# Kernel optimization log

Hardware: AMD Instinct MI355X
Metric: run time of the kernel (lower is better)

The kernel has to match this reference:

```python
import jax, jax.numpy as jnp
import numpy as np

# Faithful math: AlphaLayer(maxdim=1) builds the Delaunay complex with simplex
# filtration value = max pairwise Euclidean distance; BarcodePolyFeature(0, 2, 0)
# sums (death - birth)^2 over FINITE H0 bars. For this filtration, H0 births are
# all 0 and finite H0 deaths are exactly the Euclidean-MST edge lengths (the EMST
# is a subgraph of the Delaunay graph), so the feature equals
# sum over MST edges of squared edge length. We compute it with a vectorized
# Prim's algorithm (lax.scan over N-1 selection steps, vmapped over batch).

NCC = 2  # num_connected_components
EPS = 1e-8


def _batch_normalize(x):
    # per-sample, per-channel standardization over the points axis
    mu = x.mean(axis=1, keepdims=True)
    sd = x.std(axis=1, keepdims=True)
    return (x - mu) / (sd + EPS)


def _pairwise_sq(pts):
    # pts: [N, D] -> [N, N] squared Euclidean distances
    sq = jnp.sum(pts * pts, axis=-1)
    d2 = sq[:, None] + sq[None, :] - 2.0 * (pts @ pts.T)
    return jnp.maximum(d2, 0.0)


def _mst_sq_cost(pts):
    # sum of squared Euclidean MST edge lengths via Prim's algorithm
    d2 = _pairwise_sq(pts)          # [N, N]
    n = d2.shape[0]
    visited0 = jnp.zeros(n, dtype=bool).at[0].set(True)
    mind0 = d2[0]                   # min sq-distance from tree to each node

    def step(carry, _):
        mind, visited = carry
        masked = jnp.where(visited, jnp.inf, mind)
        j = jnp.argmin(masked)
        cost = mind[j]              # squared length of MST edge added
        visited = visited.at[j].set(True)
        mind = jnp.minimum(mind, d2[j])
        return (mind, visited), cost

    _, costs = jax.lax.scan(step, (mind0, visited0), None, length=n - 1)
    return costs.sum()


def setup_inputs() -> dict:
    key = jax.random.key(0)
    r = jax.random.normal(key, (16, 2048, 3), dtype=jnp.float32)
    return {"r": r}


def reference(r):
    chunks = jnp.split(r, NCC, axis=1)  # torch.chunk(r, dim=1, chunks=ncc)
    res = []
    for c in chunks:
        cn = _batch_normalize(c)                 # [B, N/ncc, D]
        per_sample = jax.vmap(_mst_sq_cost)(cn)  # [B]
        res.append(per_sample.mean())            # reduction='mean'
    return sum(res) / len(res)
```

## Files before the change

### kernel.cpp

```cpp
#include <hip/hip_runtime.h>
#include <math.h>
#include <stdint.h>


#define NSAMP   32
#define NPTS    1024
#define SBLK    8
#define NPN     128
#define TPB     1024
#define NROUNDS 10
#define EMPTY64 0xFFFFFFFFFFFFFFFFull

typedef unsigned long long u64;
typedef unsigned short u16;

__device__ __forceinline__ void block_sum2(float& a, float& b, float* red) {
#pragma unroll
  for (int off = 32; off > 0; off >>= 1) {
    a += __shfl_xor(a, off, 64);
    b += __shfl_xor(b, off, 64);
  }
  __syncthreads();
  const int wid = threadIdx.x >> 6;
  if ((threadIdx.x & 63) == 0) { red[wid * 2] = a; red[wid * 2 + 1] = b; }
  __syncthreads();
  float ra = 0.f, rb = 0.f;
#pragma unroll
  for (int k = 0; k < 16; ++k) { ra += red[k * 2]; rb += red[k * 2 + 1]; }
  a = ra; b = rb;
}

__device__ __forceinline__ void boruvka_scan(const float4* P, u64* Wl,
                                             int part, int tid, u64 tag) {
  const int g = tid >> 5, sl = tid & 31;
  const int n0 = part * NPN + g * 4;
  float mex[4], mey[4], mez[4]; unsigned mc[4];
#pragma unroll
  for (int n = 0; n < 4; ++n) {
    const float4 p = P[n0 + n];
    mex[n] = p.x; mey[n] = p.y; mez[n] = p.z; mc[n] = __float_as_uint(p.w);
  }
  float bd[4]; int bj[4];
#pragma unroll
  for (int n = 0; n < 4; ++n) { bd[n] = INFINITY; bj[n] = n0 + n; }
#pragma unroll 8
  for (int jj = 0; jj < 32; ++jj) {
    const int j = sl + (jj << 5);
    const float4 q = P[j];
    const unsigned qc = __float_as_uint(q.w);
#pragma unroll
    for (int n = 0; n < 4; ++n) {
      const float dx = mex[n] - q.x, dy = mey[n] - q.y, dz = mez[n] - q.z;
      float d2 = dx * dx + dy * dy + dz * dz;
      d2 = (qc == mc[n]) ? INFINITY : d2;
      if (d2 < bd[n]) { bd[n] = d2; bj[n] = j; }
    }
  }
#pragma unroll
  for (int off = 16; off > 0; off >>= 1) {
#pragma unroll
    for (int n = 0; n < 4; ++n) {
      const float od = __shfl_xor(bd[n], off, 64);
      const int   oj = __shfl_xor(bj[n], off, 64);
      if (od < bd[n] || (od == bd[n] && oj < bj[n])) { bd[n] = od; bj[n] = oj; }
    }
  }
  if (sl == 0) {
#pragma unroll
    for (int n = 0; n < 4; ++n) {
      if (bd[n] < INFINITY) {
        const int node = n0 + n, j = bj[n];
        const unsigned a = (unsigned)(node < j ? node : j);
        const unsigned b = (unsigned)(node < j ? j : node);
        const u64 key = tag | ((u64)__float_as_uint(bd[n]) << 20)
                      | (a << 10) | b;
        atomicMin(&Wl[mc[n]], key);
      }
    }
  }
}

__global__ __launch_bounds__(TPB) void topo_k0(
    const float* __restrict__ r, float4* __restrict__ pts4,
    u64* __restrict__ gw) {
  const int s = blockIdx.x & 31, part = blockIdx.x >> 5, tid = threadIdx.x;
  __shared__ float4 P[NPTS];
  __shared__ u64 Wl[NPTS];
  __shared__ float red[32];

  const float* __restrict__ base = r + (size_t)s * (NPTS * 3);
  const float px = base[tid * 3 + 0];
  const float py = base[tid * 3 + 1];
  const float pz = base[tid * 3 + 2];
  float sx = px, sy = py, sz = pz, dm = 0.f;
  block_sum2(sx, sy, red); block_sum2(sz, dm, red);
  const float mx = sx * (1.f / NPTS), my = sy * (1.f / NPTS), mz = sz * (1.f / NPTS);
  const float ex = px - mx, ey = py - my, ez = pz - mz;
  float vx = ex * ex, vy = ey * ey, vz = ez * ez;
  dm = 0.f;
  block_sum2(vx, vy, red); block_sum2(vz, dm, red);
  const float ix = 1.f / (sqrtf(vx * (1.f / NPTS)) + 1e-8f);
  const float iy = 1.f / (sqrtf(vy * (1.f / NPTS)) + 1e-8f);
  const float iz = 1.f / (sqrtf(vz * (1.f / NPTS)) + 1e-8f);
  const float4 pv =
      make_float4(ex * ix, ey * iy, ez * iz, __uint_as_float((unsigned)tid));
  P[tid] = pv;
  if (part == 0) pts4[(size_t)s * NPTS + tid] = pv;
  if (tid < NPN) {
    gw[(size_t)s * NPTS + part * NPN + tid] = EMPTY64;
    gw[(size_t)(NSAMP + s) * NPTS + part * NPN + tid] = EMPTY64;
  }
  Wl[tid] = EMPTY64;
  __syncthreads();

  boruvka_scan(P, Wl, part, tid, (u64)15 << 60);
  __syncthreads();
  const u64 w = Wl[tid];
  if (w != EMPTY64) atomicMin(&gw[(size_t)s * NPTS + tid], w);
}

__global__ __launch_bounds__(TPB) void topo_fused(
    const float4* __restrict__ pts4, u64* __restrict__ gw,
    u16* __restrict__ glab, int* __restrict__ ncomp,
    float* __restrict__ totals, int rd) {
  const int s = blockIdx.x & 31, part = blockIdx.x >> 5, tid = threadIdx.x;
  if (rd >= 2 && ncomp[s] == 1) return;
  __shared__ float4 P[NPTS];
  __shared__ u64 Wl[NPTS];
  __shared__ u16 oldlab[NPTS];
  __shared__ short parentL[NPTS];
  __shared__ float red[32];

  const u64* __restrict__ gwp =
      gw + (size_t)(((rd - 1) & 1) ? (NSAMP + s) : s) * NPTS;
  u64* __restrict__ gwc = gw + (size_t)((rd & 1) ? (NSAMP + s) : s) * NPTS;

  const float4 pc = pts4[(size_t)s * NPTS + tid];
  const u64 w = gwp[tid];
  Wl[tid] = w;
  oldlab[tid] = (rd == 1) ? (u16)tid : glab[s * NPTS + tid];
  __syncthreads();

  const unsigned curtag = (unsigned)(16 - rd);
  float wadd = 0.f;
  short par = (short)tid;
  if ((unsigned)(w >> 60) == curtag) {
    const int pmin = (int)((w >> 10) & 1023u);
    const int pmax = (int)(w & 1023u);
    const int cmin = oldlab[pmin], cmax = oldlab[pmax];
    const int c2 = (cmin == tid) ? cmax : cmin;
    par = (short)c2;
    const bool dup = (Wl[c2] == w);
    if (!dup || tid < c2)
      wadd = __uint_as_float((unsigned)((w >> 20) & 0xFFFFFFFFull));
  }
  parentL[tid] = par;
  __syncthreads();
  int c = oldlab[tid];
  {
    int prev = -1, p = c;
    for (int it = 0; it < 1024; ++it) {
      const int nx = parentL[p];
      if (nx == p) break;
      if (nx == prev) { p = p < prev ? p : prev; break; }
      prev = p; p = nx;
    }
    c = p;
  }
  float fc = (c == tid) ? 1.f : 0.f;
  block_sum2(wadd, fc, red);
  P[tid] = make_float4(pc.x, pc.y, pc.z, __uint_as_float((unsigned)c));
  if (part == 0) {
    glab[s * NPTS + tid] = (u16)c;
    if (tid == 0) {
      totals[s] = (rd == 1 ? 0.f : totals[s]) + wadd;
      ncomp[s] = (int)fc;
    }
  }
  if (fc == 1.f) return;

  Wl[tid] = EMPTY64;
  __syncthreads();
  boruvka_scan(P, Wl, part, tid, (u64)(15 - rd) << 60);
  __syncthreads();
  const u64 wn = Wl[tid];
  if (wn != EMPTY64) atomicMin(&gwc[tid], wn);
}

__global__ __launch_bounds__(64) void topo_finish(
    const float* __restrict__ totals, float* __restrict__ out) {
  float v = (threadIdx.x < NSAMP) ? totals[threadIdx.x] : 0.f;
#pragma unroll
  for (int off = 32; off > 0; off >>= 1) v += __shfl_xor(v, off, 64);
  if (threadIdx.x == 0) out[0] = v * (1.f / NSAMP);
}

extern "C" void kernel_launch(void* const* d_in, const int* in_sizes, int n_in,
                              void* d_out, int out_size, void* d_ws, size_t ws_size,
                              hipStream_t stream) {
  const float* r = (const float*)d_in[0];
  float* out = (float*)d_out;
  (void)in_sizes; (void)n_in; (void)out_size; (void)ws_size;

  char* ws = (char*)d_ws;
  float4* pts4  = (float4*)ws;
  u64*    gw    = (u64*)(ws + 524288);
  u16*    glab  = (u16*)(ws + 1048576);
  int*    ncomp = (int*)(ws + 1114112);
  float*  totals= (float*)(ws + 1118208);

  topo_k0<<<dim3(NSAMP * SBLK), dim3(TPB), 0, stream>>>(r, pts4, gw);
  for (int rd = 1; rd <= NROUNDS; ++rd) {
    topo_fused<<<dim3(NSAMP * SBLK), dim3(TPB), 0, stream>>>(
        pts4, gw, glab, ncomp, totals, rd);
  }
  topo_finish<<<dim3(1), dim3(64), 0, stream>>>(totals, out);
}
```

Measured before the change: 145.6 us.

## Compact live samples and redistribute blocks across remaining Boruvka work

Each Boruvka round now builds a compact list of samples that still have more than one component, kept in double-buffered live lists and label arrays. The next round assigns its 256 blocks only to those live samples, so fewer live samples means more blocks per sample and fewer nodes per thread group in the scan (templated NG of 4, 2 or 1). The old per-sample label shared array is folded into the P.w field. This aims to keep the GPU busy in late rounds when most samples have finished, at the cost of extra atomics, an extra sync and more template variants.

```diff
diff --git a/kernel.cpp b/kernel.cpp
--- a/kernel.cpp
+++ b/kernel.cpp
@@ -5,8 +5,6 @@
 
 #define NSAMP   32
 #define NPTS    1024
-#define SBLK    8
-#define NPN     128
 #define TPB     1024
 #define NROUNDS 10
 #define EMPTY64 0xFFFFFFFFFFFFFFFFull
@@ -30,26 +28,27 @@
   a = ra; b = rb;
 }
 
+template <int NG>
 __device__ __forceinline__ void boruvka_scan(const float4* P, u64* Wl,
                                              int part, int tid, u64 tag) {
   const int g = tid >> 5, sl = tid & 31;
-  const int n0 = part * NPN + g * 4;
-  float mex[4], mey[4], mez[4]; unsigned mc[4];
-#pragma unroll
-  for (int n = 0; n < 4; ++n) {
+  const int n0 = part * (NG * 32) + g * NG;
+  float mex[NG], mey[NG], mez[NG]; unsigned mc[NG];
+#pragma unroll
+  for (int n = 0; n < NG; ++n) {
     const float4 p = P[n0 + n];
     mex[n] = p.x; mey[n] = p.y; mez[n] = p.z; mc[n] = __float_as_uint(p.w);
   }
-  float bd[4]; int bj[4];
-#pragma unroll
-  for (int n = 0; n < 4; ++n) { bd[n] = INFINITY; bj[n] = n0 + n; }
+  float bd[NG]; int bj[NG];
+#pragma unroll
+  for (int n = 0; n < NG; ++n) { bd[n] = INFINITY; bj[n] = n0 + n; }
 #pragma unroll 8
   for (int jj = 0; jj < 32; ++jj) {
     const int j = sl + (jj << 5);
     const float4 q = P[j];
     const unsigned qc = __float_as_uint(q.w);
 #pragma unroll
-    for (int n = 0; n < 4; ++n) {
+    for (int n = 0; n < NG; ++n) {
       const float dx = mex[n] - q.x, dy = mey[n] - q.y, dz = mez[n] - q.z;
       float d2 = dx * dx + dy * dy + dz * dz;
       d2 = (qc == mc[n]) ? INFINITY : d2;
@@ -59,7 +58,7 @@
 #pragma unroll
   for (int off = 16; off > 0; off >>= 1) {
 #pragma unroll
-    for (int n = 0; n < 4; ++n) {
+    for (int n = 0; n < NG; ++n) {
       const float od = __shfl_xor(bd[n], off, 64);
       const int   oj = __shfl_xor(bj[n], off, 64);
       if (od < bd[n] || (od == bd[n] && oj < bj[n])) { bd[n] = od; bj[n] = oj; }
@@ -67,7 +66,7 @@
   }
   if (sl == 0) {
 #pragma unroll
-    for (int n = 0; n < 4; ++n) {
+    for (int n = 0; n < NG; ++n) {
       if (bd[n] < INFINITY) {
         const int node = n0 + n, j = bj[n];
         const unsigned a = (unsigned)(node < j ? node : j);
@@ -82,7 +81,8 @@
 
 __global__ __launch_bounds__(TPB) void topo_k0(
     const float* __restrict__ r, float4* __restrict__ pts4,
-    u64* __restrict__ gw) {
+    u64* __restrict__ gw, u16* __restrict__ glab0,
+    int* __restrict__ live_cnt, int* __restrict__ live_list0) {
   const int s = blockIdx.x & 31, part = blockIdx.x >> 5, tid = threadIdx.x;
   __shared__ float4 P[NPTS];
   __shared__ u64 Wl[NPTS];
@@ -105,15 +105,21 @@
   const float4 pv =
       make_float4(ex * ix, ey * iy, ez * iz, __uint_as_float((unsigned)tid));
   P[tid] = pv;
-  if (part == 0) pts4[(size_t)s * NPTS + tid] = pv;
-  if (tid < NPN) {
-    gw[(size_t)s * NPTS + part * NPN + tid] = EMPTY64;
-    gw[(size_t)(NSAMP + s) * NPTS + part * NPN + tid] = EMPTY64;
+  if (part == 0) {
+    pts4[(size_t)s * NPTS + tid] = pv;
+    glab0[s * NPTS + tid] = (u16)tid;
+    if (tid == 0) live_list0[s] = s;
+  }
+  if (blockIdx.x == 0 && tid <= NROUNDS)
+    live_cnt[tid] = (tid == 0) ? NSAMP : 0;
+  if (tid < 128) {
+    gw[(size_t)s * NPTS + part * 128 + tid] = EMPTY64;
+    gw[(size_t)(NSAMP + s) * NPTS + part * 128 + tid] = EMPTY64;
   }
   Wl[tid] = EMPTY64;
   __syncthreads();
 
-  boruvka_scan(P, Wl, part, tid, (u64)15 << 60);
+  boruvka_scan<4>(P, Wl, part, tid, (u64)15 << 60);
   __syncthreads();
   const u64 w = Wl[tid];
   if (w != EMPTY64) atomicMin(&gw[(size_t)s * NPTS + tid], w);
@@ -121,13 +127,21 @@
 
 __global__ __launch_bounds__(TPB) void topo_fused(
     const float4* __restrict__ pts4, u64* __restrict__ gw,
-    u16* __restrict__ glab, int* __restrict__ ncomp,
+    const u16* __restrict__ glab_r, u16* __restrict__ glab_w,
+    const int* __restrict__ live_cnt_prev, int* __restrict__ live_cnt_cur,
+    const int* __restrict__ live_list_prev, int* __restrict__ live_list_cur,
     float* __restrict__ totals, int rd) {
-  const int s = blockIdx.x & 31, part = blockIdx.x >> 5, tid = threadIdx.x;
-  if (rd >= 2 && ncomp[s] == 1) return;
+  const int n_live = live_cnt_prev[0];
+  if (n_live == 0) return;
+  const int bsh = (n_live <= 8) ? 5 : (n_live <= 16 ? 4 : 3);
+  const int idx = blockIdx.x >> bsh;
+  const int part = blockIdx.x & ((1 << bsh) - 1);
+  if (idx >= n_live) return;
+  const int s = live_list_prev[idx];
+  const int tid = threadIdx.x;
+
   __shared__ float4 P[NPTS];
   __shared__ u64 Wl[NPTS];
-  __shared__ u16 oldlab[NPTS];
   __shared__ short parentL[NPTS];
   __shared__ float red[32];
 
@@ -137,8 +151,9 @@
 
   const float4 pc = pts4[(size_t)s * NPTS + tid];
   const u64 w = gwp[tid];
+  const u16 ol = glab_r[s * NPTS + tid];
   Wl[tid] = w;
-  oldlab[tid] = (rd == 1) ? (u16)tid : glab[s * NPTS + tid];
+  P[tid] = make_float4(pc.x, pc.y, pc.z, __uint_as_float((unsigned)ol));
   __syncthreads();
 
   const unsigned curtag = (unsigned)(16 - rd);
@@ -147,7 +162,8 @@
   if ((unsigned)(w >> 60) == curtag) {
     const int pmin = (int)((w >> 10) & 1023u);
     const int pmax = (int)(w & 1023u);
-    const int cmin = oldlab[pmin], cmax = oldlab[pmax];
+    const int cmin = (int)__float_as_uint(P[pmin].w);
+    const int cmax = (int)__float_as_uint(P[pmax].w);
     const int c2 = (cmin == tid) ? cmax : cmin;
     par = (short)c2;
     const bool dup = (Wl[c2] == w);
@@ -156,7 +172,7 @@
   }
   parentL[tid] = par;
   __syncthreads();
-  int c = oldlab[tid];
+  int c = (int)__float_as_uint(P[tid].w);
   {
     int prev = -1, p = c;
     for (int it = 0; it < 1024; ++it) {
@@ -169,19 +185,26 @@
   }
   float fc = (c == tid) ? 1.f : 0.f;
   block_sum2(wadd, fc, red);
-  P[tid] = make_float4(pc.x, pc.y, pc.z, __uint_as_float((unsigned)c));
+  __syncthreads();
+  P[tid].w = __uint_as_float((unsigned)c);
   if (part == 0) {
-    glab[s * NPTS + tid] = (u16)c;
+    glab_w[s * NPTS + tid] = (u16)c;
     if (tid == 0) {
       totals[s] = (rd == 1 ? 0.f : totals[s]) + wadd;
-      ncomp[s] = (int)fc;
+      if (fc > 1.5f) {
+        const int pos = atomicAdd(live_cnt_cur, 1);
+        live_list_cur[pos] = s;
+      }
     }
   }
   if (fc == 1.f) return;
 
   Wl[tid] = EMPTY64;
   __syncthreads();
-  boruvka_scan(P, Wl, part, tid, (u64)(15 - rd) << 60);
+  const u64 tag = (u64)(15 - rd) << 60;
+  if (bsh == 3)      boruvka_scan<4>(P, Wl, part, tid, tag);
+  else if (bsh == 4) boruvka_scan<2>(P, Wl, part, tid, tag);
+  else               boruvka_scan<1>(P, Wl, part, tid, tag);
   __syncthreads();
   const u64 wn = Wl[tid];
   if (wn != EMPTY64) atomicMin(&gwc[tid], wn);
@@ -203,16 +226,24 @@
   (void)in_sizes; (void)n_in; (void)out_size; (void)ws_size;
 
   char* ws = (char*)d_ws;
-  float4* pts4  = (float4*)ws;
-  u64*    gw    = (u64*)(ws + 524288);
-  u16*    glab  = (u16*)(ws + 1048576);
-  int*    ncomp = (int*)(ws + 1114112);
-  float*  totals= (float*)(ws + 1118208);
-
-  topo_k0<<<dim3(NSAMP * SBLK), dim3(TPB), 0, stream>>>(r, pts4, gw);
+  float4* pts4   = (float4*)ws;
+  u64*    gw     = (u64*)(ws + 524288);
+  u16*    glabA  = (u16*)(ws + 1048576);
+  u16*    glabB  = (u16*)(ws + 1114112);
+  float*  totals = (float*)(ws + 1179648);
+  int*    live_cnt  = (int*)(ws + 1180160);
+  int*    live_list = (int*)(ws + 1180224);
+
+  topo_k0<<<dim3(NSAMP * 8), dim3(TPB), 0, stream>>>(
+      r, pts4, gw, glabA, live_cnt, live_list);
   for (int rd = 1; rd <= NROUNDS; ++rd) {
-    topo_fused<<<dim3(NSAMP * SBLK), dim3(TPB), 0, stream>>>(
-        pts4, gw, glab, ncomp, totals, rd);
+    u16* gr = ((rd - 1) & 1) ? glabB : glabA;
+    u16* gwr = (rd & 1) ? glabB : glabA;
+    topo_fused<<<dim3(256), dim3(TPB), 0, stream>>>(
+        pts4, gw, gr, gwr,
+        live_cnt + (rd - 1), live_cnt + rd,
+        live_list + (rd - 1) * NSAMP, live_list + rd * NSAMP,
+        totals, rd);
   }
   topo_finish<<<dim3(1), dim3(64), 0, stream>>>(totals, out);
 }
```

Measured after the change: 153.9 us. 5.7% more time.
